# Kernel tuning notes

Measured on AMD Instinct MI355X. Metric: run time of the kernel, lower is better.

The kernel has to match this reference:

```python
import jax, jax.numpy as jnp
import numpy as np
import math

HIDDEN = 768
N_HEADS = 12
HEAD = HIDDEN // N_HEADS


def setup_inputs() -> dict:
    key = jax.random.key(0)
    k1, k2, k3, k4, k5 = jax.random.split(key, 5)
    x = jax.random.normal(k1, (2, 2048, HIDDEN), dtype=jnp.float32)
    s = 1.0 / math.sqrt(HIDDEN)
    W_qkv = jax.random.uniform(k2, (HIDDEN, 3 * HIDDEN), minval=-s, maxval=s, dtype=jnp.float32)
    b_qkv = jax.random.uniform(k3, (3 * HIDDEN,), minval=-s, maxval=s, dtype=jnp.float32)
    W_out = jax.random.uniform(k4, (HIDDEN, HIDDEN), minval=-s, maxval=s, dtype=jnp.float32)
    b_out = jax.random.uniform(k5, (HIDDEN,), minval=-s, maxval=s, dtype=jnp.float32)
    return {"x": x, "W_qkv": W_qkv, "b_qkv": b_qkv, "W_out": W_out, "b_out": b_out}


def reference(x, W_qkv, b_qkv, W_out, b_out):
    b, n, _ = x.shape
    qkv = x @ W_qkv + b_qkv                      # [b, n, 3H]
    q, k, v = jnp.split(qkv, 3, axis=-1)
    def heads(t):
        return t.reshape(b, n, N_HEADS, HEAD).transpose(0, 2, 1, 3)  # b h n l
    q, k, v = heads(q), heads(k), heads(v)
    scores = jnp.einsum('bhql,bhkl->bhqk', q, k) / math.sqrt(HEAD)
    mask = jnp.arange(n)[:, None] < jnp.arange(n)[None, :]  # True above diagonal
    scores = jnp.where(mask, jnp.float32(-10000.0), scores)
    attn = jax.nn.softmax(scores, axis=-1)
    out = jnp.einsum('bhqk,bhkl->bhql', attn, v)
    out = out.transpose(0, 2, 1, 3).reshape(b, n, HIDDEN)
    return out @ W_out + b_out
```

## Files before the change

kernel.cpp:

```cpp
#include <hip/hip_runtime.h>

typedef __attribute__((ext_vector_type(8))) short short8;
typedef __attribute__((ext_vector_type(4))) short short4v;
typedef __attribute__((ext_vector_type(4))) float floatx4;
typedef __attribute__((ext_vector_type(16))) float floatx16;

#define HIDDEN 768
#define NH 12
#define HD 64
#define SEQ 2048
#define BATCH 2
#define BHN (BATCH*NH)
#define MTOT (BATCH*SEQ)
#define NQKV (3*HIDDEN)
#define QSCALE 0.1803368801111204f

__device__ __forceinline__ short f2bf(float f) {
  union { float f; unsigned u; } v; v.f = f;
  unsigned r = v.u + 0x7FFFu + ((v.u >> 16) & 1u);
  return (short)(r >> 16);
}
__device__ __forceinline__ unsigned bfrne(float f) {
  unsigned u = __float_as_uint(f);
  return u + 0x7FFFu + ((u >> 16) & 1u);
}
__device__ __forceinline__ unsigned pk2(float a, float b) {
  return __builtin_amdgcn_perm(bfrne(b), bfrne(a), 0x07060302u);
}
__device__ __forceinline__ float bf2f(short s) {
  return __uint_as_float(((unsigned)(unsigned short)s) << 16);
}
__device__ __forceinline__ floatx4 mfma_bf16(short8 a, short8 b, floatx4 c) {
  return __builtin_amdgcn_mfma_f32_16x16x32_bf16(a, b, c, 0, 0, 0);
}
__device__ __forceinline__ floatx16 mfma32(short8 a, short8 b, floatx16 c) {
  return __builtin_amdgcn_mfma_f32_32x32x16_bf16(a, b, c, 0, 0, 0);
}
__device__ __forceinline__ short8 ld8(const short* p) {
  return *reinterpret_cast<const short8*>(p);
}
__device__ __forceinline__ void glds16(const short* g, short* l) {
  __builtin_amdgcn_global_load_lds(
      (const __attribute__((address_space(1))) void*)g,
      (__attribute__((address_space(3))) void*)l, 16, 0, 0);
}

__global__ __launch_bounds__(256) void transpose_cvt(const float* __restrict__ W,
                                                     short* __restrict__ WT,
                                                     int K, int N) {
  __shared__ short t[64][72];
  int nb = blockIdx.x * 64, kb = blockIdx.y * 64;
  int tid = threadIdx.x;
  {
    int k  = tid >> 2;
    int n0 = (tid & 3) << 4;
    const float4* src = reinterpret_cast<const float4*>(W + (size_t)(kb + k) * N + nb + n0);
    #pragma unroll
    for (int c = 0; c < 4; ++c) {
      float4 v = src[c];
      t[n0 + c*4 + 0][k] = f2bf(v.x);
      t[n0 + c*4 + 1][k] = f2bf(v.y);
      t[n0 + c*4 + 2][k] = f2bf(v.z);
      t[n0 + c*4 + 3][k] = f2bf(v.w);
    }
  }
  __syncthreads();
  {
    int n  = tid >> 2;
    int k0 = (tid & 3) << 4;
    const short8* row = reinterpret_cast<const short8*>(&t[n][k0]);
    short8* dst = reinterpret_cast<short8*>(WT + (size_t)(nb + n) * K + kb + k0);
    dst[0] = row[0];
    dst[1] = row[1];
  }
}

__global__ __launch_bounds__(256) void cvt_x(const float* __restrict__ X,
                                             short* __restrict__ Xb) {
  int i = (blockIdx.x * 256 + threadIdx.x) * 8;
  const float4* s = reinterpret_cast<const float4*>(X + i);
  float4 v0 = s[0], v1 = s[1];
  short8 o;
  o[0] = f2bf(v0.x); o[1] = f2bf(v0.y); o[2] = f2bf(v0.z); o[3] = f2bf(v0.w);
  o[4] = f2bf(v1.x); o[5] = f2bf(v1.y); o[6] = f2bf(v1.z); o[7] = f2bf(v1.w);
  *reinterpret_cast<short8*>(Xb + i) = o;
}

__global__ __launch_bounds__(256) void gemm_qkv(const short* __restrict__ Xb,
                                                const short* __restrict__ WT,
                                                const float* __restrict__ bias,
                                                short* __restrict__ Qb,
                                                short* __restrict__ Kb,
                                                short* __restrict__ VTb) {
  __shared__ short As[128 * 32];
  __shared__ short Bs[128 * 32];
  int m0 = blockIdx.x * 128, n0 = blockIdx.y * 128;
  int tid = threadIdx.x;
  int lane = tid & 63, wv = tid >> 6;
  int wm = (wv >> 1) << 6, wn = (wv & 1) << 6;
  int quad = lane >> 4, l16 = lane & 15;

  int srow = lane >> 2;
  int schunk = (lane & 3) ^ ((lane >> 3) & 3);
  const short* ag0 = Xb + (size_t)(m0 + wv * 32 + srow) * HIDDEN + schunk * 8;
  const short* ag1 = ag0 + 16 * HIDDEN;
  const short* bg0 = WT + (size_t)(n0 + wv * 32 + srow) * HIDDEN + schunk * 8;
  const short* bg1 = bg0 + 16 * HIDDEN;
  short* lA0 = As + wv * 1024;
  short* lB0 = Bs + wv * 1024;

  int sw = ((l16 >> 1) & 3);
  int aoff = (wm + l16) * 32 + ((quad ^ sw) << 3);
  int boff = (wn + l16) * 32 + ((quad ^ sw) << 3);

  floatx4 acc[4][4] = {};
  for (int kk = 0; kk < HIDDEN; kk += 32) {
    __syncthreads();
    glds16(ag0, lA0);
    glds16(ag1, lA0 + 512);
    glds16(bg0, lB0);
    glds16(bg1, lB0 + 512);
    ag0 += 32; ag1 += 32; bg0 += 32; bg1 += 32;
    __syncthreads();
    short8 af[4], bfr[4];
    #pragma unroll
    for (int i = 0; i < 4; ++i)
      af[i] = *reinterpret_cast<const short8*>(&As[aoff + i * 512]);
    #pragma unroll
    for (int j = 0; j < 4; ++j)
      bfr[j] = *reinterpret_cast<const short8*>(&Bs[boff + j * 512]);
    #pragma unroll
    for (int i = 0; i < 4; ++i)
      #pragma unroll
      for (int j = 0; j < 4; ++j)
        acc[i][j] = mfma_bf16(af[i], bfr[j], acc[i][j]);
  }
  int colbase = n0 + wn;
  int part = colbase / HIDDEN;
  #pragma unroll
  for (int j = 0; j < 4; ++j) {
    int col = colbase + j * 16 + l16;
    float bs = bias[col];
    int rem = col - part * HIDDEN;
    int h = rem >> 6, d = rem & 63;
    #pragma unroll
    for (int i = 0; i < 4; ++i) {
      #pragma unroll
      for (int r = 0; r < 4; ++r) {
        int row = m0 + wm + i * 16 + quad * 4 + r;
        float v = acc[i][j][r] + bs;
        int bb = row >> 11, s = row & 2047;
        int bh = bb * NH + h;
        if (part == 0) {
          Qb[((size_t)bh * SEQ + s) * HD + d] = f2bf(v * QSCALE);
        } else if (part == 1) {
          Kb[((size_t)bh * SEQ + s) * HD + d] = f2bf(v);
        } else {
          VTb[((size_t)bh * HD + d) * SEQ + s] = f2bf(v);
        }
      }
    }
  }
}

__global__ __launch_bounds__(256, 4) void attn_partial(const short* __restrict__ Qb,
                                                       const short* __restrict__ Kb,
                                                       const short* __restrict__ VTb,
                                                       short* __restrict__ PO,
                                                       float* __restrict__ PM,
                                                       float* __restrict__ PL) {
  __shared__ __align__(16) char lds[32768];
  int blk = blockIdx.x;
  int cls = blk & 7;
  int j   = blk >> 3;
  int headsel = j / 40;
  int bh  = cls + 8 * headsel;
  int cidx = 39 - (j - headsel * 40);
  int qt, c;
  if (cidx < 4)       { qt = cidx;                  c = 0; }
  else if (cidx < 12) { qt = 4 + ((cidx - 4) >> 1); c = (cidx - 4) & 1; }
  else if (cidx < 24) { int t = cidx - 12; int q3 = t / 3; qt = 8 + q3; c = t - 3 * q3; }
  else                { int t = cidx - 24; qt = 12 + (t >> 2); c = t & 3; }
  int g = qt >> 2, p = qt & 3;
  int idx = bh * 40 + (g + 1) * (2 * g + p) + c;

  int nt  = 2 * qt + 2;
  int kt0 = c * 8;
  int kt1 = min(nt, kt0 + 8);
  int qb0 = qt * 128;

  int tid = threadIdx.x;
  int lane = tid & 63, wv = tid >> 6;
  int l31 = lane & 31, h = lane >> 5, x = lane & 7;
  const short* Qp = Qb + (size_t)bh * SEQ * HD;
  const short* Kp = Kb + (size_t)bh * SEQ * HD;
  const short* Vp = VTb + (size_t)bh * HD * SEQ;

  int qs  = qb0 + wv * 32 + l31;
  int qlo = qb0 + wv * 32;
  int qhi = qlo + 31;

  short8 bq[4];
  #pragma unroll
  for (int dc = 0; dc < 4; ++dc)
    bq[dc] = ld8(Qp + qs * HD + dc * 16 + h * 8);

  int sr = tid >> 2, scg = tid & 3;
  const short* kg = Kp + (kt0 * 64 + sr) * HD + scg * 16;
  const short* vg = Vp + (size_t)sr * SEQ + kt0 * 64 + scg * 16;
  int wbase = (sr << 7) | (((scg << 1) ^ (sr & 7)) << 4);

  int rbase[4];
  #pragma unroll
  for (int kc = 0; kc < 4; ++kc)
    rbase[kc] = (l31 << 7) | ((((kc << 1) | h) ^ x) << 4);

  {
    short8 k0 = ld8(kg), k1 = ld8(kg + 8);
    short8 v0 = ld8(vg), v1 = ld8(vg + 8);
    *reinterpret_cast<short8*>(lds + wbase)                = k0;
    *reinterpret_cast<short8*>(lds + (wbase ^ 16))         = k1;
    *reinterpret_cast<short8*>(lds + 16384 + wbase)        = v0;
    *reinterpret_cast<short8*>(lds + 16384 + (wbase ^ 16)) = v1;
  }
  __syncthreads();

  floatx16 o0 = {}, o1 = {};
  float m_run = -1e30f, l_run = 0.f;

  for (int kt = kt0; kt < kt1; ++kt) {
    int cur = (kt - kt0) & 1;
    int curK = cur * 8192, curV = 16384 + cur * 8192;
    int kb = kt * 64;
    bool have_next = (kt + 1 < kt1);

    short8 nk0, nk1, nv0, nv1;
    if (have_next) {
      kg += 64 * HD; vg += 64;
      nk0 = ld8(kg); nk1 = ld8(kg + 8);
      nv0 = ld8(vg); nv1 = ld8(vg + 8);
    }

    if (kb <= qhi) {
      floatx16 s0 = {}, s1 = {};
      #pragma unroll
      for (int kc = 0; kc < 4; ++kc) {
        short8 ka0 = *reinterpret_cast<const short8*>(lds + curK + rbase[kc]);
        short8 ka1 = *reinterpret_cast<const short8*>(lds + curK + 4096 + rbase[kc]);
        s0 = mfma32(ka0, bq[kc], s0);
        s1 = mfma32(ka1, bq[kc], s1);
      }
      if (kb + 63 > qlo) {
        #pragma unroll
        for (int r = 0; r < 16; ++r) {
          int kvr = kb + (r & 3) + 8 * (r >> 2) + 4 * h;
          s0[r] = (kvr > qs) ? -1e30f : s0[r];
          s1[r] = (kvr + 32 > qs) ? -1e30f : s1[r];
        }
      }
      float mloc = m_run;
      #pragma unroll
      for (int r = 0; r < 16; ++r) { mloc = fmaxf(mloc, s0[r]); mloc = fmaxf(mloc, s1[r]); }
      mloc = fmaxf(mloc, __shfl_xor(mloc, 32));
      float m_new = mloc;
      float alpha = __builtin_amdgcn_exp2f(m_run - m_new);
      float sloc = 0.f;
      #pragma unroll
      for (int r = 0; r < 16; ++r) {
        s0[r] = __builtin_amdgcn_exp2f(s0[r] - m_new); sloc += s0[r];
        s1[r] = __builtin_amdgcn_exp2f(s1[r] - m_new); sloc += s1[r];
      }
      sloc += __shfl_xor(sloc, 32);
      l_run = l_run * alpha + sloc;
      m_run = m_new;
      o0 *= alpha; o1 *= alpha;
      short8 pb[4];
      #pragma unroll
      for (int kvc = 0; kvc < 4; ++kvc) {
        int base = (kvc & 1) * 8;
        const floatx16& P = (kvc < 2) ? s0 : s1;
        unsigned e0 = pk2(P[base + 0], P[base + 1]);
        unsigned e1 = pk2(P[base + 2], P[base + 3]);
        unsigned f0 = pk2(P[base + 4], P[base + 5]);
        unsigned f1 = pk2(P[base + 6], P[base + 7]);
        unsigned k_0 = h ? f0 : e0, k_1 = h ? f1 : e1;
        unsigned s_0 = h ? e0 : f0, s_1 = h ? e1 : f1;
        unsigned r_0 = __shfl_xor((int)s_0, 32);
        unsigned r_1 = __shfl_xor((int)s_1, 32);
        union { unsigned u[4]; short8 v; } pbu;
        pbu.u[0] = h ? r_0 : k_0;
        pbu.u[1] = h ? r_1 : k_1;
        pbu.u[2] = h ? k_0 : r_0;
        pbu.u[3] = h ? k_1 : r_1;
        pb[kvc] = pbu.v;
      }
      #pragma unroll
      for (int kvc = 0; kvc < 4; ++kvc) {
        short8 va0 = *reinterpret_cast<const short8*>(lds + curV + rbase[kvc]);
        short8 va1 = *reinterpret_cast<const short8*>(lds + curV + 4096 + rbase[kvc]);
        o0 = mfma32(va0, pb[kvc], o0);
        o1 = mfma32(va1, pb[kvc], o1);
      }
    }

    if (have_next) {
      int nK = (cur ^ 1) * 8192, nV = 16384 + (cur ^ 1) * 8192;
      *reinterpret_cast<short8*>(lds + nK + wbase)        = nk0;
      *reinterpret_cast<short8*>(lds + nK + (wbase ^ 16)) = nk1;
      *reinterpret_cast<short8*>(lds + nV + wbase)        = nv0;
      *reinterpret_cast<short8*>(lds + nV + (wbase ^ 16)) = nv1;
    }
    __syncthreads();
  }

  int qloc = wv * 32 + l31;
  size_t pobase = (size_t)idx * 8192 + qloc * 64;
  #pragma unroll
  for (int dt = 0; dt < 2; ++dt) {
    #pragma unroll
    for (int cc = 0; cc < 4; ++cc) {
      int d = dt * 32 + 8 * cc + 4 * h;
      short4v w;
      #pragma unroll
      for (int r = 0; r < 4; ++r)
        w[r] = f2bf(dt ? o1[4 * cc + r] : o0[4 * cc + r]);
      *reinterpret_cast<short4v*>(PO + pobase + d) = w;
    }
  }
  if (h == 0) {
    PM[idx * 128 + qloc] = m_run;
    PL[idx * 128 + qloc] = l_run;
  }
}

__global__ __launch_bounds__(256) void attn_merge(const short* __restrict__ PO,
                                                  const float* __restrict__ PM,
                                                  const float* __restrict__ PL,
                                                  short* __restrict__ AO) {
  int blk = blockIdx.x;
  int bh = blk >> 4, qt = blk & 15;
  int g = qt >> 2, p = qt & 3;
  int base = bh * 40 + (g + 1) * (2 * g + p);
  int nc = g + 1;
  int tid = threadIdx.x;
  int q = tid >> 1, dh = (tid & 1) << 5;
  float mv[4];
  float M = -1e30f;
  for (int c = 0; c < nc; ++c) {
    mv[c] = PM[(base + c) * 128 + q];
    M = fmaxf(M, mv[c]);
  }
  float wsum = 0.f;
  float acc[32] = {};
  for (int c = 0; c < nc; ++c) {
    float w = __builtin_amdgcn_exp2f(mv[c] - M);
    wsum += PL[(base + c) * 128 + q] * w;
    const short8* po = reinterpret_cast<const short8*>(PO + (size_t)(base + c) * 8192 + q * 64 + dh);
    #pragma unroll
    for (int k = 0; k < 4; ++k) {
      short8 v = po[k];
      #pragma unroll
      for (int e = 0; e < 8; ++e)
        acc[k * 8 + e] += w * bf2f(v[e]);
    }
  }
  float inv = 1.f / wsum;
  int b = bh / NH, hh = bh % NH;
  int s = qt * 128 + q;
  short* dst = AO + ((size_t)(b * SEQ + s)) * HIDDEN + hh * HD + dh;
  #pragma unroll
  for (int k = 0; k < 4; ++k) {
    short8 w8;
    #pragma unroll
    for (int e = 0; e < 8; ++e)
      w8[e] = f2bf(acc[k * 8 + e] * inv);
    *reinterpret_cast<short8*>(dst + k * 8) = w8;
  }
}

__global__ __launch_bounds__(256) void gemm_out(const short* __restrict__ AO,
                                                const short* __restrict__ WT,
                                                const float* __restrict__ bias,
                                                float* __restrict__ out) {
  __shared__ short As[128 * 32];
  __shared__ short Bs[128 * 32];
  int m0 = blockIdx.x * 128, n0 = blockIdx.y * 128;
  int tid = threadIdx.x;
  int lane = tid & 63, wv = tid >> 6;
  int wm = (wv >> 1) << 6, wn = (wv & 1) << 6;
  int quad = lane >> 4, l16 = lane & 15;

  int srow = lane >> 2;
  int schunk = (lane & 3) ^ ((lane >> 3) & 3);
  const short* ag0 = AO + (size_t)(m0 + wv * 32 + srow) * HIDDEN + schunk * 8;
  const short* ag1 = ag0 + 16 * HIDDEN;
  const short* bg0 = WT + (size_t)(n0 + wv * 32 + srow) * HIDDEN + schunk * 8;
  const short* bg1 = bg0 + 16 * HIDDEN;
  short* lA0 = As + wv * 1024;
  short* lB0 = Bs + wv * 1024;

  int sw = ((l16 >> 1) & 3);
  int aoff = (wm + l16) * 32 + ((quad ^ sw) << 3);
  int boff = (wn + l16) * 32 + ((quad ^ sw) << 3);

  floatx4 acc[4][4] = {};
  for (int kk = 0; kk < HIDDEN; kk += 32) {
    __syncthreads();
    glds16(ag0, lA0);
    glds16(ag1, lA0 + 512);
    glds16(bg0, lB0);
    glds16(bg1, lB0 + 512);
    ag0 += 32; ag1 += 32; bg0 += 32; bg1 += 32;
    __syncthreads();
    short8 af[4], bfr[4];
    #pragma unroll
    for (int i = 0; i < 4; ++i)
      af[i] = *reinterpret_cast<const short8*>(&As[aoff + i * 512]);
    #pragma unroll
    for (int j = 0; j < 4; ++j)
      bfr[j] = *reinterpret_cast<const short8*>(&Bs[boff + j * 512]);
    #pragma unroll
    for (int i = 0; i < 4; ++i)
      #pragma unroll
      for (int j = 0; j < 4; ++j)
        acc[i][j] = mfma_bf16(af[i], bfr[j], acc[i][j]);
  }
  #pragma unroll
  for (int j = 0; j < 4; ++j) {
    int col = n0 + wn + j * 16 + l16;
    float bs = bias[col];
    #pragma unroll
    for (int i = 0; i < 4; ++i) {
      #pragma unroll
      for (int r = 0; r < 4; ++r) {
        int row = m0 + wm + i * 16 + quad * 4 + r;
        out[(size_t)row * HIDDEN + col] = acc[i][j][r] + bs;
      }
    }
  }
}

extern "C" void kernel_launch(void* const* d_in, const int* in_sizes, int n_in,
                              void* d_out, int out_size, void* d_ws, size_t ws_size,
                              hipStream_t stream) {
  const float* x    = (const float*)d_in[0];
  const float* Wqkv = (const float*)d_in[1];
  const float* bqkv = (const float*)d_in[2];
  const float* Wout = (const float*)d_in[3];
  const float* bout = (const float*)d_in[4];
  float* out = (float*)d_out;

  short* WqkvT = (short*)d_ws;
  short* WoutT = WqkvT + (size_t)NQKV * HIDDEN;
  short* Qb    = WoutT + (size_t)HIDDEN * HIDDEN;
  short* Kb    = Qb + (size_t)BHN * SEQ * HD;
  short* VTb   = Kb + (size_t)BHN * SEQ * HD;
  short* AO    = VTb + (size_t)BHN * SEQ * HD;
  short* Xb    = AO + (size_t)MTOT * HIDDEN;
  short* PO    = Xb;
  float* PM    = (float*)(PO + (size_t)960 * 8192);
  float* PL    = PM + 960 * 128;

  cvt_x<<<dim3(MTOT * HIDDEN / (256 * 8)), 256, 0, stream>>>(x, Xb);
  transpose_cvt<<<dim3(NQKV / 64, HIDDEN / 64), 256, 0, stream>>>(Wqkv, WqkvT, HIDDEN, NQKV);
  transpose_cvt<<<dim3(HIDDEN / 64, HIDDEN / 64), 256, 0, stream>>>(Wout, WoutT, HIDDEN, HIDDEN);
  gemm_qkv<<<dim3(MTOT / 128, NQKV / 128), 256, 0, stream>>>(Xb, WqkvT, bqkv, Qb, Kb, VTb);
  attn_partial<<<dim3(960), 256, 0, stream>>>(Qb, Kb, VTb, PO, PM, PL);
  attn_merge<<<dim3(BHN * 16), 256, 0, stream>>>(PO, PM, PL, AO);
  gemm_out<<<dim3(MTOT / 128, HIDDEN / 128), 256, 0, stream>>>(AO, WoutT, bout, out);
}
```

Measured before the change: 163.3 us.

## Fuse prep kernels, use direct-to-LDS loads in attention, shrink out-GEMM tile

Merges the x conversion and both weight transpose-convert kernels into one launch, which removes two kernel launch gaps. In the attention kernel, K/V tiles are now prefetched with global_load_lds straight into the next LDS buffer instead of going through registers. This frees VGPRs and drops the separate LDS store phase, with a new per-wave row layout and XOR swizzle. The output GEMM uses 64-row M tiles, doubling its block count to fill more CUs at the cost of less reuse of the B tile.

New measurement: 157.2 us. -3.8%, faster.

```diff
diff --git a/kernel.cpp b/kernel.cpp
--- a/kernel.cpp
+++ b/kernel.cpp
@@ -45,11 +45,30 @@
       (__attribute__((address_space(3))) void*)l, 16, 0, 0);
 }
 
-__global__ __launch_bounds__(256) void transpose_cvt(const float* __restrict__ W,
-                                                     short* __restrict__ WT,
-                                                     int K, int N) {
+__global__ __launch_bounds__(256) void prep(const float* __restrict__ X,
+                                            const float* __restrict__ Wqkv,
+                                            const float* __restrict__ Wout,
+                                            short* __restrict__ Xb,
+                                            short* __restrict__ WqkvT,
+                                            short* __restrict__ WoutT) {
   __shared__ short t[64][72];
-  int nb = blockIdx.x * 64, kb = blockIdx.y * 64;
+  int bx = blockIdx.x;
+  if (bx < 1536) {
+    int i = (bx * 256 + threadIdx.x) * 8;
+    const float4* s = reinterpret_cast<const float4*>(X + i);
+    float4 v0 = s[0], v1 = s[1];
+    short8 o;
+    o[0] = f2bf(v0.x); o[1] = f2bf(v0.y); o[2] = f2bf(v0.z); o[3] = f2bf(v0.w);
+    o[4] = f2bf(v1.x); o[5] = f2bf(v1.y); o[6] = f2bf(v1.z); o[7] = f2bf(v1.w);
+    *reinterpret_cast<short8*>(Xb + i) = o;
+    return;
+  }
+  int tt = bx - 1536;
+  int bxx = tt % 48, by = tt / 48;
+  const float* W; short* WT; int N; int nb;
+  if (bxx < 36) { W = Wqkv; WT = WqkvT; N = NQKV;   nb = bxx * 64; }
+  else          { W = Wout; WT = WoutT; N = HIDDEN; nb = (bxx - 36) * 64; }
+  int kb = by * 64;
   int tid = threadIdx.x;
   {
     int k  = tid >> 2;
@@ -69,21 +88,10 @@
     int n  = tid >> 2;
     int k0 = (tid & 3) << 4;
     const short8* row = reinterpret_cast<const short8*>(&t[n][k0]);
-    short8* dst = reinterpret_cast<short8*>(WT + (size_t)(nb + n) * K + kb + k0);
+    short8* dst = reinterpret_cast<short8*>(WT + (size_t)(nb + n) * HIDDEN + kb + k0);
     dst[0] = row[0];
     dst[1] = row[1];
   }
-}
-
-__global__ __launch_bounds__(256) void cvt_x(const float* __restrict__ X,
-                                             short* __restrict__ Xb) {
-  int i = (blockIdx.x * 256 + threadIdx.x) * 8;
-  const float4* s = reinterpret_cast<const float4*>(X + i);
-  float4 v0 = s[0], v1 = s[1];
-  short8 o;
-  o[0] = f2bf(v0.x); o[1] = f2bf(v0.y); o[2] = f2bf(v0.z); o[3] = f2bf(v0.w);
-  o[4] = f2bf(v1.x); o[5] = f2bf(v1.y); o[6] = f2bf(v1.z); o[7] = f2bf(v1.w);
-  *reinterpret_cast<short8*>(Xb + i) = o;
 }
 
 __global__ __launch_bounds__(256) void gemm_qkv(const short* __restrict__ Xb,
@@ -205,24 +213,21 @@
   for (int dc = 0; dc < 4; ++dc)
     bq[dc] = ld8(Qp + qs * HD + dc * 16 + h * 8);
 
-  int sr = tid >> 2, scg = tid & 3;
-  const short* kg = Kp + (kt0 * 64 + sr) * HD + scg * 16;
-  const short* vg = Vp + (size_t)sr * SEQ + kt0 * 64 + scg * 16;
-  int wbase = (sr << 7) | (((scg << 1) ^ (sr & 7)) << 4);
+  int lr = lane >> 3;
+  int cgc = (lane & 7) ^ lr;
+  const short* kgl = Kp + (size_t)(kt0 * 64 + wv * 16 + lr) * HD + cgc * 8;
+  const short* vgl = Vp + (size_t)(wv * 16 + lr) * SEQ + kt0 * 64 + cgc * 8;
+  int wofs = wv * 2048;
 
   int rbase[4];
   #pragma unroll
   for (int kc = 0; kc < 4; ++kc)
     rbase[kc] = (l31 << 7) | ((((kc << 1) | h) ^ x) << 4);
 
-  {
-    short8 k0 = ld8(kg), k1 = ld8(kg + 8);
-    short8 v0 = ld8(vg), v1 = ld8(vg + 8);
-    *reinterpret_cast<short8*>(lds + wbase)                = k0;
-    *reinterpret_cast<short8*>(lds + (wbase ^ 16))         = k1;
-    *reinterpret_cast<short8*>(lds + 16384 + wbase)        = v0;
-    *reinterpret_cast<short8*>(lds + 16384 + (wbase ^ 16)) = v1;
-  }
+  glds16(kgl,            (short*)(lds + wofs));
+  glds16(kgl + 8 * HD,   (short*)(lds + wofs + 1024));
+  glds16(vgl,            (short*)(lds + 16384 + wofs));
+  glds16(vgl + 8 * SEQ,  (short*)(lds + 16384 + wofs + 1024));
   __syncthreads();
 
   floatx16 o0 = {}, o1 = {};
@@ -232,13 +237,14 @@
     int cur = (kt - kt0) & 1;
     int curK = cur * 8192, curV = 16384 + cur * 8192;
     int kb = kt * 64;
-    bool have_next = (kt + 1 < kt1);
-
-    short8 nk0, nk1, nv0, nv1;
-    if (have_next) {
-      kg += 64 * HD; vg += 64;
-      nk0 = ld8(kg); nk1 = ld8(kg + 8);
-      nv0 = ld8(vg); nv1 = ld8(vg + 8);
+
+    if (kt + 1 < kt1) {
+      kgl += 64 * HD; vgl += 64;
+      int nK = (cur ^ 1) * 8192, nV = 16384 + (cur ^ 1) * 8192;
+      glds16(kgl,           (short*)(lds + nK + wofs));
+      glds16(kgl + 8 * HD,  (short*)(lds + nK + wofs + 1024));
+      glds16(vgl,           (short*)(lds + nV + wofs));
+      glds16(vgl + 8 * SEQ, (short*)(lds + nV + wofs + 1024));
     }
 
     if (kb <= qhi) {
@@ -302,14 +308,6 @@
         o1 = mfma32(va1, pb[kvc], o1);
       }
     }
-
-    if (have_next) {
-      int nK = (cur ^ 1) * 8192, nV = 16384 + (cur ^ 1) * 8192;
-      *reinterpret_cast<short8*>(lds + nK + wbase)        = nk0;
-      *reinterpret_cast<short8*>(lds + nK + (wbase ^ 16)) = nk1;
-      *reinterpret_cast<short8*>(lds + nV + wbase)        = nv0;
-      *reinterpret_cast<short8*>(lds + nV + (wbase ^ 16)) = nv1;
-    }
     __syncthreads();
   }
 
@@ -382,45 +380,44 @@
                                                 const short* __restrict__ WT,
                                                 const float* __restrict__ bias,
                                                 float* __restrict__ out) {
-  __shared__ short As[128 * 32];
+  __shared__ short As[64 * 32];
   __shared__ short Bs[128 * 32];
-  int m0 = blockIdx.x * 128, n0 = blockIdx.y * 128;
+  int m0 = blockIdx.x * 64, n0 = blockIdx.y * 128;
   int tid = threadIdx.x;
   int lane = tid & 63, wv = tid >> 6;
-  int wm = (wv >> 1) << 6, wn = (wv & 1) << 6;
+  int wm = (wv >> 1) << 5;
+  int wn = (wv & 1) << 6;
   int quad = lane >> 4, l16 = lane & 15;
 
   int srow = lane >> 2;
   int schunk = (lane & 3) ^ ((lane >> 3) & 3);
-  const short* ag0 = AO + (size_t)(m0 + wv * 32 + srow) * HIDDEN + schunk * 8;
-  const short* ag1 = ag0 + 16 * HIDDEN;
+  const short* ag  = AO + (size_t)(m0 + wv * 16 + srow) * HIDDEN + schunk * 8;
   const short* bg0 = WT + (size_t)(n0 + wv * 32 + srow) * HIDDEN + schunk * 8;
   const short* bg1 = bg0 + 16 * HIDDEN;
-  short* lA0 = As + wv * 1024;
+  short* lA  = As + wv * 512;
   short* lB0 = Bs + wv * 1024;
 
   int sw = ((l16 >> 1) & 3);
   int aoff = (wm + l16) * 32 + ((quad ^ sw) << 3);
   int boff = (wn + l16) * 32 + ((quad ^ sw) << 3);
 
-  floatx4 acc[4][4] = {};
+  floatx4 acc[2][4] = {};
   for (int kk = 0; kk < HIDDEN; kk += 32) {
     __syncthreads();
-    glds16(ag0, lA0);
-    glds16(ag1, lA0 + 512);
+    glds16(ag, lA);
     glds16(bg0, lB0);
     glds16(bg1, lB0 + 512);
-    ag0 += 32; ag1 += 32; bg0 += 32; bg1 += 32;
+    ag += 32; bg0 += 32; bg1 += 32;
     __syncthreads();
-    short8 af[4], bfr[4];
-    #pragma unroll
-    for (int i = 0; i < 4; ++i)
+    short8 af[2], bfr[4];
+    #pragma unroll
+    for (int i = 0; i < 2; ++i)
       af[i] = *reinterpret_cast<const short8*>(&As[aoff + i * 512]);
     #pragma unroll
     for (int j = 0; j < 4; ++j)
       bfr[j] = *reinterpret_cast<const short8*>(&Bs[boff + j * 512]);
     #pragma unroll
-    for (int i = 0; i < 4; ++i)
+    for (int i = 0; i < 2; ++i)
       #pragma unroll
       for (int j = 0; j < 4; ++j)
         acc[i][j] = mfma_bf16(af[i], bfr[j], acc[i][j]);
@@ -430,7 +427,7 @@
     int col = n0 + wn + j * 16 + l16;
     float bs = bias[col];
     #pragma unroll
-    for (int i = 0; i < 4; ++i) {
+    for (int i = 0; i < 2; ++i) {
       #pragma unroll
       for (int r = 0; r < 4; ++r) {
         int row = m0 + wm + i * 16 + quad * 4 + r;
@@ -461,11 +458,9 @@
   float* PM    = (float*)(PO + (size_t)960 * 8192);
   float* PL    = PM + 960 * 128;
 
-  cvt_x<<<dim3(MTOT * HIDDEN / (256 * 8)), 256, 0, stream>>>(x, Xb);
-  transpose_cvt<<<dim3(NQKV / 64, HIDDEN / 64), 256, 0, stream>>>(Wqkv, WqkvT, HIDDEN, NQKV);
-  transpose_cvt<<<dim3(HIDDEN / 64, HIDDEN / 64), 256, 0, stream>>>(Wout, WoutT, HIDDEN, HIDDEN);
+  prep<<<dim3(2112), 256, 0, stream>>>(x, Wqkv, Wout, Xb, WqkvT, WoutT);
   gemm_qkv<<<dim3(MTOT / 128, NQKV / 128), 256, 0, stream>>>(Xb, WqkvT, bqkv, Qb, Kb, VTb);
   attn_partial<<<dim3(960), 256, 0, stream>>>(Qb, Kb, VTb, PO, PM, PL);
   attn_merge<<<dim3(BHN * 16), 256, 0, stream>>>(PO, PM, PL, AO);
-  gemm_out<<<dim3(MTOT / 128, HIDDEN / 128), 256, 0, stream>>>(AO, WoutT, bout, out);
-}
+  gemm_out<<<dim3(MTOT / 64, HIDDEN / 128), 256, 0, stream>>>(AO, WoutT, bout, out);
+}
```
